# Optimization experiments

Hardware: AMD Instinct MI355X
Metric: run time of the kernel (lower is better)

The kernel has to match this reference:

```python
import jax, jax.numpy as jnp
import numpy as np
from itertools import permutations

# NOTE: the original torch code has `loss_m = loss_r = loss_i = []`, so all three
# names alias ONE list; RI_loss = 2*sum(L) and Mag_loss = sum(L), giving a total
# of 3*sum(per-speaker r+i+mag losses)/num_spks. We reproduce that factor of 3.

def reference(masks, mixture_real, mixture_imag, target_real, target_imag, input_sizes):
    S, B, M, W, F, T, _ = masks.shape
    filt = jax.lax.complex(masks[..., 0], masks[..., 1])          # [S,B,M,W,F,T]
    mix = jax.lax.complex(mixture_real, mixture_imag)             # [S,B,M,F,T]
    ref_ch = 0
    tgt = jax.lax.complex(target_real[:, :, ref_ch], target_imag[:, :, ref_ch])  # [S,B,F,T]

    # filtering(): unfold W time-shifted copies (zero padded) then MAC over (m,w)
    p = (W - 1) // 2
    mix_pad = jnp.pad(mix, ((0, 0), (0, 0), (0, 0), (0, 0), (p, p)))
    win = jnp.stack([mix_pad[..., w:w + T] for w in range(W)], axis=3)  # [S,B,M,W,F,T]
    out = jnp.einsum('sbmwft,sbmwft->sbft', win, filt)            # [S,B,F,T] complex

    # filtering output is permutation-invariant: build pairwise loss matrix once
    d = tgt[None, :] - out[:, None]                               # [S_out, S_tgt, B, F, T]
    lr = jnp.sum(jnp.abs(d.real), axis=(-1, -2))                  # [S,S,B]
    li = jnp.sum(jnp.abs(d.imag), axis=(-1, -2))
    lm = jnp.sum(jnp.abs(jnp.abs(tgt[None, :]) - jnp.abs(out[:, None])), axis=(-1, -2))
    L = lr + li + lm                                              # [S,S,B]

    perms = list(permutations(range(S)))
    pscore = jnp.stack([3.0 * sum(L[s, pm[s]] for s in range(S)) / S for pm in perms])  # [P,B]
    min_perutt = jnp.min(pscore, axis=0)                          # [B]
    num_utts = input_sizes.shape[0]
    return jnp.sum(min_perutt) / num_utts


def setup_inputs() -> dict:
    key = jax.random.key(0)
    ks = jax.random.split(key, 6)
    S, B, M, W, F, T, C = 2, 4, 4, 3, 257, 512, 4
    masks = jax.random.normal(ks[0], (S, B, M, W, F, T, 2), dtype=jnp.float32)
    mixture_real = jax.random.normal(ks[1], (S, B, M, F, T), dtype=jnp.float32)
    mixture_imag = jax.random.normal(ks[2], (S, B, M, F, T), dtype=jnp.float32)
    target_real = jax.random.normal(ks[3], (S, B, C, F, T), dtype=jnp.float32)
    target_imag = jax.random.normal(ks[4], (S, B, C, F, T), dtype=jnp.float32)
    input_sizes = jax.random.randint(ks[5], (B,), 1, 512).astype(jnp.int64)
    return {"masks": masks, "mixture_real": mixture_real, "mixture_imag": mixture_imag,
            "target_real": target_real, "target_imag": target_imag, "input_sizes": input_sizes}
```

## Files before the change

### kernel.cpp

```cpp
#include <hip/hip_runtime.h>

#define S_SPK 2
#define B_BATCH 4
#define M_MIC 4
#define W_TAP 3
#define F_FREQ 257
#define T_TIME 512
#define C_CH 4
#define FT (F_FREQ * T_TIME)

#define NBLK_X 65
#define NBLK_Y 32
#define NSLOT (NBLK_X * NBLK_Y)

typedef float float4u __attribute__((ext_vector_type(4), aligned(4)));
typedef float float2a __attribute__((ext_vector_type(2), aligned(8)));

#define AS1 __attribute__((address_space(1)))
#define AS3 __attribute__((address_space(3)))


__global__ __launch_bounds__(256) void pit_main_kernel(
    const float* __restrict__ masks,
    const float* __restrict__ mixr,
    const float* __restrict__ mixi,
    const float* __restrict__ tgtr,
    const float* __restrict__ tgti,
    float* __restrict__ ws)
{
    const int sb   = blockIdx.y >> 2;
    const int tq   = blockIdx.y & 3;
    const int b    = sb & 3;
    const int wave = threadIdx.x >> 6;
    const int lane = threadIdx.x & 63;

    const int f    = blockIdx.x * 4 + wave;
    const int fc   = (f < F_FREQ) ? f : (F_FREQ - 1);
    const float vf = (f < F_FREQ) ? 1.0f : 0.0f;

    const int t0 = tq * 128 + (lane << 1);
    const long rowBase = (long)fc * T_TIME;
    const long mixSB   = (long)sb * M_MIC * FT + rowBase;
    const long mskSB   = (long)sb * M_MIC;

    __shared__ float lmask[4][M_MIC * W_TAP][256];

    #pragma unroll
    for (int m = 0; m < M_MIC; ++m) {
        #pragma unroll
        for (int w = 0; w < W_TAP; ++w) {
            const float* srow = masks +
                ((((mskSB + m) * W_TAP + w) * F_FREQ + fc) * (long)T_TIME + tq * 128) * 2
                + (lane << 2);
            __builtin_amdgcn_global_load_lds(
                (const AS1 void*)srow,
                (AS3 void*)&lmask[wave][m * W_TAP + w][0],
                16, 0, 0);
        }
    }

    int tc = t0 - 1;
    tc = tc < 0 ? 0 : tc;
    tc = tc > (T_TIME - 4) ? (T_TIME - 4) : tc;

    float4u wr[M_MIC], wi[M_MIC];
    #pragma unroll
    for (int m = 0; m < M_MIC; ++m) {
        wr[m] = *(const float4u*)(mixr + mixSB + (long)m * FT + tc);
        wi[m] = *(const float4u*)(mixi + mixSB + (long)m * FT + tc);
    }

    const long tOff = rowBase + t0;
    const float2a t0r = *(const float2a*)(tgtr + ((long)(0 * B_BATCH + b) * C_CH) * FT + tOff);
    const float2a t0i = *(const float2a*)(tgti + ((long)(0 * B_BATCH + b) * C_CH) * FT + tOff);
    const float2a t1r = *(const float2a*)(tgtr + ((long)(1 * B_BATCH + b) * C_CH) * FT + tOff);
    const float2a t1i = *(const float2a*)(tgti + ((long)(1 * B_BATCH + b) * C_CH) * FT + tOff);

    if (t0 == 0) {
        #pragma unroll
        for (int m = 0; m < M_MIC; ++m) {
            wr[m][3] = wr[m][2]; wr[m][2] = wr[m][1]; wr[m][1] = wr[m][0]; wr[m][0] = 0.0f;
            wi[m][3] = wi[m][2]; wi[m][2] = wi[m][1]; wi[m][1] = wi[m][0]; wi[m][0] = 0.0f;
        }
    } else if (t0 == T_TIME - 2) {
        #pragma unroll
        for (int m = 0; m < M_MIC; ++m) {
            wr[m][0] = wr[m][1]; wr[m][1] = wr[m][2]; wr[m][2] = wr[m][3]; wr[m][3] = 0.0f;
            wi[m][0] = wi[m][1]; wi[m][1] = wi[m][2]; wi[m][2] = wi[m][3]; wi[m][3] = 0.0f;
        }
    }

    asm volatile("s_waitcnt vmcnt(0)" ::: "memory");

    float or0 = 0.f, oi0 = 0.f, or1 = 0.f, oi1 = 0.f;
    #pragma unroll
    for (int m = 0; m < M_MIC; ++m) {
        #pragma unroll
        for (int w = 0; w < W_TAP; ++w) {
            const float4 qq = *(const float4*)&lmask[wave][m * W_TAP + w][lane << 2];
            or0 += wr[m][w]     * qq.x - wi[m][w]     * qq.y;
            oi0 += wr[m][w]     * qq.y + wi[m][w]     * qq.x;
            or1 += wr[m][w + 1] * qq.z - wi[m][w + 1] * qq.w;
            oi1 += wr[m][w + 1] * qq.w + wi[m][w + 1] * qq.z;
        }
    }

    const float ao0 = sqrtf(or0 * or0 + oi0 * oi0);
    const float ao1 = sqrtf(or1 * or1 + oi1 * oi1);
    const float a00 = sqrtf(t0r[0] * t0r[0] + t0i[0] * t0i[0]);
    const float a01 = sqrtf(t0r[1] * t0r[1] + t0i[1] * t0i[1]);
    const float a10 = sqrtf(t1r[0] * t1r[0] + t1i[0] * t1i[0]);
    const float a11 = sqrtf(t1r[1] * t1r[1] + t1i[1] * t1i[1]);

    float L0 = fabsf(t0r[0] - or0) + fabsf(t0i[0] - oi0) + fabsf(a00 - ao0)
             + fabsf(t0r[1] - or1) + fabsf(t0i[1] - oi1) + fabsf(a01 - ao1);
    float L1 = fabsf(t1r[0] - or0) + fabsf(t1i[0] - oi0) + fabsf(a10 - ao0)
             + fabsf(t1r[1] - or1) + fabsf(t1i[1] - oi1) + fabsf(a11 - ao1);
    L0 *= vf;
    L1 *= vf;

    #pragma unroll
    for (int off = 32; off > 0; off >>= 1) {
        L0 += __shfl_down(L0, off, 64);
        L1 += __shfl_down(L1, off, 64);
    }
    __shared__ float s0[4], s1[4];
    if (lane == 0) { s0[wave] = L0; s1[wave] = L1; }
    __syncthreads();
    if (threadIdx.x == 0) {
        const int slot = blockIdx.y * NBLK_X + blockIdx.x;
        ws[slot * 2 + 0] = s0[0] + s0[1] + s0[2] + s0[3];
        ws[slot * 2 + 1] = s1[0] + s1[1] + s1[2] + s1[3];
    }
}

__global__ __launch_bounds__(256) void pit_final_kernel(
    const float* __restrict__ ws, float* __restrict__ out, int num_utts)
{
    float acc[16];
    #pragma unroll
    for (int i = 0; i < 16; ++i) acc[i] = 0.0f;

    for (int slot = threadIdx.x; slot < NSLOT; slot += 256) {
        const int y  = slot / NBLK_X;
        const int sb = y >> 2;
        const int so = sb >> 2;
        const int b  = sb & 3;
        acc[((so * 2 + 0) << 2) + b] += ws[slot * 2 + 0];
        acc[((so * 2 + 1) << 2) + b] += ws[slot * 2 + 1];
    }

    __shared__ float red[16][4];
    const int wave = threadIdx.x >> 6;
    const int lane = threadIdx.x & 63;
    #pragma unroll
    for (int i = 0; i < 16; ++i) {
        float v = acc[i];
        #pragma unroll
        for (int off = 32; off > 0; off >>= 1) v += __shfl_down(v, off, 64);
        if (lane == 0) red[i][wave] = v;
    }
    __syncthreads();

    if (threadIdx.x == 0) {
        float L[16];
        #pragma unroll
        for (int i = 0; i < 16; ++i) L[i] = red[i][0] + red[i][1] + red[i][2] + red[i][3];
        float accu = 0.0f;
        for (int b = 0; b < B_BATCH; ++b) {
            const float pid = L[(0 * 2 + 0) * 4 + b] + L[(1 * 2 + 1) * 4 + b];
            const float psw = L[(0 * 2 + 1) * 4 + b] + L[(1 * 2 + 0) * 4 + b];
            const float sc0 = 3.0f * pid / (float)S_SPK;
            const float sc1 = 3.0f * psw / (float)S_SPK;
            accu += fminf(sc0, sc1);
        }
        out[0] = accu / (float)num_utts;
    }
}

extern "C" void kernel_launch(void* const* d_in, const int* in_sizes, int n_in,
                              void* d_out, int out_size, void* d_ws, size_t ws_size,
                              hipStream_t stream) {
    const float* masks = (const float*)d_in[0];
    const float* mixr  = (const float*)d_in[1];
    const float* mixi  = (const float*)d_in[2];
    const float* tgtr  = (const float*)d_in[3];
    const float* tgti  = (const float*)d_in[4];
    const int num_utts = in_sizes[5];

    float* ws  = (float*)d_ws;
    float* out = (float*)d_out;

    dim3 grid(NBLK_X, NBLK_Y);
    pit_main_kernel<<<grid, 256, 0, stream>>>(masks, mixr, mixi, tgtr, tgti, ws);

    pit_final_kernel<<<1, 256, 0, stream>>>(ws, out, num_utts);
}
```

Before: 200.7 us.

## Loop over time quarters per block with register double-buffered mask loads

Each block now covers all four time quarters of a frequency row, cutting the grid from 32 to 8 rows of blocks. Mask loads go straight into a two-stage register buffer that prefetches the next quarter while the current one is computed, replacing the LDS async loads and the full vmcnt wait. This is meant to hide memory latency and cut per-block overhead. In exchange it launches fewer blocks (520), which may lower occupancy and raise register pressure from 24 float4 mask registers.

```diff
diff --git a/kernel.cpp b/kernel.cpp
--- a/kernel.cpp
+++ b/kernel.cpp
@@ -10,14 +10,11 @@
 #define FT (F_FREQ * T_TIME)
 
 #define NBLK_X 65
-#define NBLK_Y 32
+#define NBLK_Y 8
 #define NSLOT (NBLK_X * NBLK_Y)
 
 typedef float float4u __attribute__((ext_vector_type(4), aligned(4)));
 typedef float float2a __attribute__((ext_vector_type(2), aligned(8)));
-
-#define AS1 __attribute__((address_space(1)))
-#define AS3 __attribute__((address_space(3)))
 
 
 __global__ __launch_bounds__(256) void pit_main_kernel(
@@ -28,8 +25,7 @@
     const float* __restrict__ tgti,
     float* __restrict__ ws)
 {
-    const int sb   = blockIdx.y >> 2;
-    const int tq   = blockIdx.y & 3;
+    const int sb   = blockIdx.y;
     const int b    = sb & 3;
     const int wave = threadIdx.x >> 6;
     const int lane = threadIdx.x & 63;
@@ -38,84 +34,90 @@
     const int fc   = (f < F_FREQ) ? f : (F_FREQ - 1);
     const float vf = (f < F_FREQ) ? 1.0f : 0.0f;
 
-    const int t0 = tq * 128 + (lane << 1);
     const long rowBase = (long)fc * T_TIME;
     const long mixSB   = (long)sb * M_MIC * FT + rowBase;
-    const long mskSB   = (long)sb * M_MIC;
 
-    __shared__ float lmask[4][M_MIC * W_TAP][256];
+    const float* mbase = masks + ((long)(sb * 12) * F_FREQ + fc) * (T_TIME * 2)
+                       + (lane << 2);
+    const long MW_STRIDE = (long)F_FREQ * T_TIME * 2;
+
+    const long tg0 = (long)(0 * B_BATCH + b) * C_CH * FT + rowBase;
+    const long tg1 = (long)(1 * B_BATCH + b) * C_CH * FT + rowBase;
+
+    float L0 = 0.0f, L1 = 0.0f;
+
+    float4 qb[2][12];
+    #pragma unroll
+    for (int mw = 0; mw < 12; ++mw)
+        qb[0][mw] = *(const float4*)(mbase + (long)mw * MW_STRIDE);
 
     #pragma unroll
-    for (int m = 0; m < M_MIC; ++m) {
+    for (int c = 0; c < 4; ++c) {
+        if (c < 3) {
+            #pragma unroll
+            for (int mw = 0; mw < 12; ++mw)
+                qb[(c + 1) & 1][mw] =
+                    *(const float4*)(mbase + (long)mw * MW_STRIDE + (c + 1) * 256);
+        }
+
+        const int t0 = c * 128 + (lane << 1);
+
+        int tc = t0 - 1;
+        tc = tc < 0 ? 0 : tc;
+        tc = tc > (T_TIME - 4) ? (T_TIME - 4) : tc;
+
+        float4u wr[M_MIC], wi[M_MIC];
         #pragma unroll
-        for (int w = 0; w < W_TAP; ++w) {
-            const float* srow = masks +
-                ((((mskSB + m) * W_TAP + w) * F_FREQ + fc) * (long)T_TIME + tq * 128) * 2
-                + (lane << 2);
-            __builtin_amdgcn_global_load_lds(
-                (const AS1 void*)srow,
-                (AS3 void*)&lmask[wave][m * W_TAP + w][0],
-                16, 0, 0);
+        for (int m = 0; m < M_MIC; ++m) {
+            wr[m] = *(const float4u*)(mixr + mixSB + (long)m * FT + tc);
+            wi[m] = *(const float4u*)(mixi + mixSB + (long)m * FT + tc);
         }
+
+        const float2a t0r = *(const float2a*)(tgtr + tg0 + t0);
+        const float2a t0i = *(const float2a*)(tgti + tg0 + t0);
+        const float2a t1r = *(const float2a*)(tgtr + tg1 + t0);
+        const float2a t1i = *(const float2a*)(tgti + tg1 + t0);
+
+        if (t0 == 0) {
+            #pragma unroll
+            for (int m = 0; m < M_MIC; ++m) {
+                wr[m][3]=wr[m][2]; wr[m][2]=wr[m][1]; wr[m][1]=wr[m][0]; wr[m][0]=0.f;
+                wi[m][3]=wi[m][2]; wi[m][2]=wi[m][1]; wi[m][1]=wi[m][0]; wi[m][0]=0.f;
+            }
+        } else if (t0 == T_TIME - 2) {
+            #pragma unroll
+            for (int m = 0; m < M_MIC; ++m) {
+                wr[m][0]=wr[m][1]; wr[m][1]=wr[m][2]; wr[m][2]=wr[m][3]; wr[m][3]=0.f;
+                wi[m][0]=wi[m][1]; wi[m][1]=wi[m][2]; wi[m][2]=wi[m][3]; wi[m][3]=0.f;
+            }
+        }
+
+        float or0 = 0.f, oi0 = 0.f, or1 = 0.f, oi1 = 0.f;
+        #pragma unroll
+        for (int m = 0; m < M_MIC; ++m) {
+            #pragma unroll
+            for (int w = 0; w < W_TAP; ++w) {
+                const float4 qq = qb[c & 1][m * W_TAP + w];
+                or0 += wr[m][w]     * qq.x - wi[m][w]     * qq.y;
+                oi0 += wr[m][w]     * qq.y + wi[m][w]     * qq.x;
+                or1 += wr[m][w + 1] * qq.z - wi[m][w + 1] * qq.w;
+                oi1 += wr[m][w + 1] * qq.w + wi[m][w + 1] * qq.z;
+            }
+        }
+
+        const float ao0 = sqrtf(or0 * or0 + oi0 * oi0);
+        const float ao1 = sqrtf(or1 * or1 + oi1 * oi1);
+        const float a00 = sqrtf(t0r[0] * t0r[0] + t0i[0] * t0i[0]);
+        const float a01 = sqrtf(t0r[1] * t0r[1] + t0i[1] * t0i[1]);
+        const float a10 = sqrtf(t1r[0] * t1r[0] + t1i[0] * t1i[0]);
+        const float a11 = sqrtf(t1r[1] * t1r[1] + t1i[1] * t1i[1]);
+
+        L0 += fabsf(t0r[0] - or0) + fabsf(t0i[0] - oi0) + fabsf(a00 - ao0)
+            + fabsf(t0r[1] - or1) + fabsf(t0i[1] - oi1) + fabsf(a01 - ao1);
+        L1 += fabsf(t1r[0] - or0) + fabsf(t1i[0] - oi0) + fabsf(a10 - ao0)
+            + fabsf(t1r[1] - or1) + fabsf(t1i[1] - oi1) + fabsf(a11 - ao1);
     }
 
-    int tc = t0 - 1;
-    tc = tc < 0 ? 0 : tc;
-    tc = tc > (T_TIME - 4) ? (T_TIME - 4) : tc;
-
-    float4u wr[M_MIC], wi[M_MIC];
-    #pragma unroll
-    for (int m = 0; m < M_MIC; ++m) {
-        wr[m] = *(const float4u*)(mixr + mixSB + (long)m * FT + tc);
-        wi[m] = *(const float4u*)(mixi + mixSB + (long)m * FT + tc);
-    }
-
-    const long tOff = rowBase + t0;
-    const float2a t0r = *(const float2a*)(tgtr + ((long)(0 * B_BATCH + b) * C_CH) * FT + tOff);
-    const float2a t0i = *(const float2a*)(tgti + ((long)(0 * B_BATCH + b) * C_CH) * FT + tOff);
-    const float2a t1r = *(const float2a*)(tgtr + ((long)(1 * B_BATCH + b) * C_CH) * FT + tOff);
-    const float2a t1i = *(const float2a*)(tgti + ((long)(1 * B_BATCH + b) * C_CH) * FT + tOff);
-
-    if (t0 == 0) {
-        #pragma unroll
-        for (int m = 0; m < M_MIC; ++m) {
-            wr[m][3] = wr[m][2]; wr[m][2] = wr[m][1]; wr[m][1] = wr[m][0]; wr[m][0] = 0.0f;
-            wi[m][3] = wi[m][2]; wi[m][2] = wi[m][1]; wi[m][1] = wi[m][0]; wi[m][0] = 0.0f;
-        }
-    } else if (t0 == T_TIME - 2) {
-        #pragma unroll
-        for (int m = 0; m < M_MIC; ++m) {
-            wr[m][0] = wr[m][1]; wr[m][1] = wr[m][2]; wr[m][2] = wr[m][3]; wr[m][3] = 0.0f;
-            wi[m][0] = wi[m][1]; wi[m][1] = wi[m][2]; wi[m][2] = wi[m][3]; wi[m][3] = 0.0f;
-        }
-    }
-
-    asm volatile("s_waitcnt vmcnt(0)" ::: "memory");
-
-    float or0 = 0.f, oi0 = 0.f, or1 = 0.f, oi1 = 0.f;
-    #pragma unroll
-    for (int m = 0; m < M_MIC; ++m) {
-        #pragma unroll
-        for (int w = 0; w < W_TAP; ++w) {
-            const float4 qq = *(const float4*)&lmask[wave][m * W_TAP + w][lane << 2];
-            or0 += wr[m][w]     * qq.x - wi[m][w]     * qq.y;
-            oi0 += wr[m][w]     * qq.y + wi[m][w]     * qq.x;
-            or1 += wr[m][w + 1] * qq.z - wi[m][w + 1] * qq.w;
-            oi1 += wr[m][w + 1] * qq.w + wi[m][w + 1] * qq.z;
-        }
-    }
-
-    const float ao0 = sqrtf(or0 * or0 + oi0 * oi0);
-    const float ao1 = sqrtf(or1 * or1 + oi1 * oi1);
-    const float a00 = sqrtf(t0r[0] * t0r[0] + t0i[0] * t0i[0]);
-    const float a01 = sqrtf(t0r[1] * t0r[1] + t0i[1] * t0i[1]);
-    const float a10 = sqrtf(t1r[0] * t1r[0] + t1i[0] * t1i[0]);
-    const float a11 = sqrtf(t1r[1] * t1r[1] + t1i[1] * t1i[1]);
-
-    float L0 = fabsf(t0r[0] - or0) + fabsf(t0i[0] - oi0) + fabsf(a00 - ao0)
-             + fabsf(t0r[1] - or1) + fabsf(t0i[1] - oi1) + fabsf(a01 - ao1);
-    float L1 = fabsf(t1r[0] - or0) + fabsf(t1i[0] - oi0) + fabsf(a10 - ao0)
-             + fabsf(t1r[1] - or1) + fabsf(t1i[1] - oi1) + fabsf(a11 - ao1);
     L0 *= vf;
     L1 *= vf;
 
@@ -142,8 +144,7 @@
     for (int i = 0; i < 16; ++i) acc[i] = 0.0f;
 
     for (int slot = threadIdx.x; slot < NSLOT; slot += 256) {
-        const int y  = slot / NBLK_X;
-        const int sb = y >> 2;
+        const int sb = slot / NBLK_X;
         const int so = sb >> 2;
         const int b  = sb & 3;
         acc[((so * 2 + 0) << 2) + b] += ws[slot * 2 + 0];
```

New measurement: 210.0 us. +4.6%, slower.
